# Performance work log

Measured on AMD Instinct MI355X. Metric: run time of the kernel, lower is better.

Reference implementation:

```python
import jax, jax.numpy as jnp
import numpy as np

B, S, H, D = 256, 512, 512, 1  # batch, seq_len, rnn_hid_size (== S*D), input_dim


def lstm_cell(x, h, c, Wih, Whh, bih, bhh):
    # torch.nn.LSTMCell: gates ordered i, f, g, o
    g = x @ Wih.T + bih + h @ Whh.T + bhh  # [B, 4H]
    i, f, gg, o = jnp.split(g, 4, axis=-1)
    i = jax.nn.sigmoid(i)
    f = jax.nn.sigmoid(f)
    gg = jnp.tanh(gg)
    o = jax.nn.sigmoid(o)
    c_new = f * c + i * gg
    h_new = o * jnp.tanh(c_new)
    return h_new, c_new


def setup_inputs() -> dict:
    key = jax.random.key(0)
    ks = jax.random.split(key, 14)
    sc = 1.0 / np.sqrt(H)  # torch LSTMCell/Linear default uniform bound
    u = lambda k, shape: jax.random.uniform(k, shape, jnp.float32, -sc, sc)
    values = jax.random.normal(ks[0], (B, S), jnp.float32)
    masks = jax.random.randint(ks[1], (B, S), 0, 2).astype(jnp.float32)
    return {
        "values": values,
        "masks": masks,
        "Wih_f": u(ks[2], (4 * H, D)), "Whh_f": u(ks[3], (4 * H, H)),
        "bih_f": u(ks[4], (4 * H,)), "bhh_f": u(ks[5], (4 * H,)),
        "Wih_b": u(ks[6], (4 * H, D)), "Whh_b": u(ks[7], (4 * H, H)),
        "bih_b": u(ks[8], (4 * H,)), "bhh_b": u(ks[9], (4 * H,)),
        "W_imp": u(ks[10], (D, H)), "b_imp": u(ks[11], (D,)),
    }


def reference(values, masks, Wih_f, Whh_f, bih_f, bhh_f,
              Wih_b, Whh_b, bih_b, bhh_b, W_imp, b_imp):
    x_f = values[:, :, None]  # [B, S, 1]
    m_f = masks[:, :, None]
    # flip over axis 2 (size 1) is a no-op, matching the original exactly
    x_b = jnp.flip(x_f, axis=2)
    m_b = jnp.flip(m_f, axis=2)

    start_f = jnp.full((B, D), 128.0, jnp.float32)
    start_b = jnp.full((B, D), -128.0, jnp.float32)
    z = jnp.zeros((B, H), jnp.float32)
    h_f, c_f = lstm_cell(start_f, z, z, Wih_f, Whh_f, bih_f, bhh_f)
    h_b, c_b = lstm_cell(start_b, z, z, Wih_b, Whh_b, bih_b, bhh_b)

    xs = (jnp.swapaxes(x_f, 0, 1), jnp.swapaxes(m_f, 0, 1),
          jnp.swapaxes(x_b, 0, 1), jnp.swapaxes(m_b, 0, 1))  # [S, B, 1] each

    def step(carry, inp):
        hf, cf, hb, cb = carry
        xf, mf, xb, mb = inp
        imp_f = hf @ W_imp.T + b_imp
        imp_b = hb @ W_imp.T + b_imp
        cc_f = (1.0 - mf) * xf + mf * imp_f
        cc_b = (1.0 - mb) * xb + mb * imp_b
        hf, cf = lstm_cell(cc_f, hf, cf, Wih_f, Whh_f, bih_f, bhh_f)
        hb, cb = lstm_cell(cc_b, hb, cb, Wih_b, Whh_b, bih_b, bhh_b)
        return (hf, cf, hb, cb), None

    (h_f, c_f, h_b, c_b), _ = jax.lax.scan(step, (h_f, c_f, h_b, c_b), xs)
    h = h_f + h_b  # [B, H]
    imputations = h.reshape(B, S, D)  # requires H == S * D
    out = imputations * (1.0 - m_f) + x_f * m_f
    return h, out
```

## Files before the change

kernel.cpp:

```cpp
#include <hip/hip_runtime.h>
#include <stdint.h>

#define B_ 256
#define S_ 512
#define H_ 512

#define XM_STRIDE 513
#define LDS_BYTES 56320

typedef __attribute__((ext_vector_type(4))) float f32x4;
typedef __attribute__((ext_vector_type(4))) int   i32x4;
typedef __attribute__((ext_vector_type(8))) short s16x8;

__device__ __forceinline__ short f2bf(float f) {
    union { float f; uint32_t u; } c; c.f = f;
    uint32_t u = c.u;
    u += 0x7fffu + ((u >> 16) & 1u);
    return (short)(u >> 16);
}
__device__ __forceinline__ float bflo(uint32_t u) { return __builtin_bit_cast(float, u << 16); }
__device__ __forceinline__ float bfhi(uint32_t u) { return __builtin_bit_cast(float, u & 0xffff0000u); }
__device__ __forceinline__ float sig_(float x)  { return 1.0f / (1.0f + __expf(-x)); }
__device__ __forceinline__ float tanh_(float x) { return 1.0f - 2.0f / (1.0f + __expf(2.0f * x)); }

__device__ __forceinline__ uint32_t pklo(uint32_t hi, uint32_t lo) {
    return __builtin_amdgcn_perm(hi, lo, 0x05040100u);
}

__device__ __forceinline__ void load_a8_issue(const void* p, i32x4* a) {
    asm volatile(
        "global_load_dwordx4 %0, %8, off sc0 sc1\n\t"
        "global_load_dwordx4 %1, %8, off offset:16 sc0 sc1\n\t"
        "global_load_dwordx4 %2, %8, off offset:128 sc0 sc1\n\t"
        "global_load_dwordx4 %3, %8, off offset:144 sc0 sc1\n\t"
        "global_load_dwordx4 %4, %8, off offset:256 sc0 sc1\n\t"
        "global_load_dwordx4 %5, %8, off offset:272 sc0 sc1\n\t"
        "global_load_dwordx4 %6, %8, off offset:384 sc0 sc1\n\t"
        "global_load_dwordx4 %7, %8, off offset:400 sc0 sc1"
        : "=&v"(a[0]), "=&v"(a[1]), "=&v"(a[2]), "=&v"(a[3]),
          "=&v"(a[4]), "=&v"(a[5]), "=&v"(a[6]), "=&v"(a[7])
        : "v"(p)
        : "memory");
}
#define AWAIT(imm, x0, x1, x2, x3) \
    asm volatile("s_waitcnt vmcnt(" #imm ")" : "+v"(x0), "+v"(x1), "+v"(x2), "+v"(x3) :: "memory")

__device__ __forceinline__ uint32_t minof8(const i32x4* ar) {
    uint32_t mn = 0xffffffffu;
    #pragma unroll
    for (int j = 0; j < 8; ++j) {
        uint32_t u0 = (uint32_t)ar[j][0], u1 = (uint32_t)ar[j][1];
        uint32_t u2 = (uint32_t)ar[j][2], u3 = (uint32_t)ar[j][3];
        uint32_t m0 = u0 < u1 ? u0 : u1;
        uint32_t m1 = u2 < u3 ? u2 : u3;
        uint32_t mm = m0 < m1 ? m0 : m1;
        mn = mn < mm ? mn : mm;
    }
    return mn;
}

__device__ __forceinline__ void group_revalidate(i32x4* ar, const void* gb, uint32_t tgtv) {
    uint32_t mn = minof8(ar);
    while (__ballot(mn >= tgtv) != ~0ull) {
        __builtin_amdgcn_s_sleep(1);
        load_a8_issue(gb, ar);
        AWAIT(0, ar[0], ar[1], ar[2], ar[3]);
        AWAIT(0, ar[4], ar[5], ar[6], ar[7]);
        mn = minof8(ar);
    }
}

__global__ void __launch_bounds__(128, 1)
lstm_kernel(const float* __restrict__ values, const float* __restrict__ masks,
            const float* __restrict__ Wih_f, const float* __restrict__ Whh_f,
            const float* __restrict__ bih_f, const float* __restrict__ bhh_f,
            const float* __restrict__ Wih_b, const float* __restrict__ Whh_b,
            const float* __restrict__ bih_b, const float* __restrict__ bhh_b,
            const float* __restrict__ W_imp, const float* __restrict__ b_imp,
            uint32_t* h_buf, float* hfin)
{
    extern __shared__ char smem_raw[];
    short*    imp_lds = (short*)smem_raw;
    uint32_t* xm_lds  = (uint32_t*)(smem_raw + 16384);

    const int tid  = threadIdx.x;
    const int lane = tid & 63;
    const int nw   = tid >> 6;

    const int bid = blockIdx.x;
    const int g   = bid & 15;
    const int w   = (bid >> 4) & 15;
    const int d   = bid >> 8;

    const float* Whh = d ? Whh_b : Whh_f;
    const float* Wih = d ? Wih_b : Wih_f;
    const float* bih = d ? bih_b : bih_f;
    const float* bhh = d ? bhh_b : bhh_f;

    const int col16 = lane & 15;
    const int koff4 = lane >> 4;
    const int jcol  = w * 32 + nw * 16 + col16;

    for (int c = tid; c < 1024; c += 128) {
        int ckoff = (c >> 4) & 3, ckb = c >> 6;
        int k0 = ckb * 32 + ckoff * 8;
        short* dst = &imp_lds[c * 8];
        #pragma unroll
        for (int j = 0; j < 8; ++j) dst[j] = f2bf(W_imp[k0 + j]);
    }
    for (int i = tid; i < 16 * 512; i += 128) {
        int r = i >> 9, s = i & 511;
        float x = values[(g * 16 + r) * S_ + s];
        float m = masks[(g * 16 + r) * S_ + s];
        float a = x * (1.0f - m);
        xm_lds[r * XM_STRIDE + s] =
            (uint32_t)(uint16_t)f2bf(a) | ((uint32_t)(uint16_t)f2bf(m) << 16);
    }

    s16x8 bfr[4][16];
    {
        const float* base = Whh + (size_t)jcol * 512 + koff4 * 8;
        #pragma unroll
        for (int gg = 0; gg < 4; ++gg) {
            const float* src = base + (size_t)gg * 512 * 512;
            #pragma unroll
            for (int kb = 0; kb < 16; ++kb) {
                f32x4 v0 = *(const f32x4*)(src + kb * 32);
                f32x4 v1 = *(const f32x4*)(src + kb * 32 + 4);
                s16x8 b;
                b[0] = f2bf(v0[0]); b[1] = f2bf(v0[1]); b[2] = f2bf(v0[2]); b[3] = f2bf(v0[3]);
                b[4] = f2bf(v1[0]); b[5] = f2bf(v1[1]); b[6] = f2bf(v1[2]); b[7] = f2bf(v1[3]);
                bfr[gg][kb] = b;
            }
        }
    }

    float bias[4], wih[4];
    #pragma unroll
    for (int gg = 0; gg < 4; ++gg) {
        int gc = gg * 512 + jcol;
        bias[gg] = bih[gc] + bhh[gc];
        wih[gg]  = Wih[gc];
    }
    const float bimp  = b_imp[0];
    const float start = d ? -128.0f : 128.0f;

    const int arow    = g * 16 + col16;
    const int rowloc  = koff4 * 4;
    const int rowbase = g * 16 + rowloc;
    const int imp_off = (koff4 * 16 + col16) * 8;

    __syncthreads();

    float c_reg[4];
    {
        float pre[4];
        #pragma unroll
        for (int gg = 0; gg < 4; ++gg) pre[gg] = start * wih[gg] + bias[gg];
        float i0 = sig_(pre[0]), g0 = tanh_(pre[2]), o0 = sig_(pre[3]);
        float c0 = i0 * g0;
        float h0 = o0 * tanh_(c0);
        #pragma unroll
        for (int r = 0; r < 4; ++r) c_reg[r] = c0;
        uint32_t dwi = (1u << 16) | (uint32_t)(uint16_t)f2bf(h0);
        char* dst = (char*)(h_buf + (size_t)d * (B_ * H_) + (size_t)rowbase * H_ + jcol);
        #pragma unroll
        for (int r = 0; r < 4; ++r)
            asm volatile("global_store_dword %0, %1, off sc0 sc1"
                         :: "v"(dst + r * 2048), "v"(dwi) : "memory");
    }

    for (int t = 0; t < S_; ++t) {
        const int p = t & 1;
        const uint32_t* hb_r = h_buf + (size_t)p       * (2 * B_ * H_) + (size_t)d * (B_ * H_);
        uint32_t*       hb_w = h_buf + (size_t)(p ^ 1) * (2 * B_ * H_) + (size_t)d * (B_ * H_);

        const uint32_t tgtv = (uint32_t)(t + 1) << 16;

        {
            const uint32_t* cp = hb_r + (size_t)(g * 16) * H_ + (lane & 31) * 16;
            for (;;) {
                uint32_t f;
                asm volatile("global_load_dword %0, %1, off sc0 sc1\n\ts_waitcnt vmcnt(0)"
                             : "=v"(f) : "v"(cp) : "memory");
                if (__ballot(f >= tgtv) == ~0ull) break;
                __builtin_amdgcn_s_sleep(2);
            }
        }

        const char* ab = (const char*)(hb_r + (size_t)arow * H_ + koff4 * 8);
        i32x4 ar0[8], ar1[8], ar2[8], ar3[8];
        load_a8_issue(ab,        ar0);
        load_a8_issue(ab + 512,  ar1);
        load_a8_issue(ab + 1024, ar2);
        load_a8_issue(ab + 1536, ar3);

        f32x4 acc0 = {0,0,0,0}, acc1 = {0,0,0,0}, acc2 = {0,0,0,0}, acc3 = {0,0,0,0};
        f32x4 acc4 = {0,0,0,0};

        #define PACK_MFMA(G, AR)                                                   \
            _Pragma("unroll")                                                      \
            for (int kk = 0; kk < 4; ++kk) {                                       \
                i32x4 pk;                                                          \
                pk[0] = (int)pklo((uint32_t)AR[2*kk  ][1], (uint32_t)AR[2*kk  ][0]); \
                pk[1] = (int)pklo((uint32_t)AR[2*kk  ][3], (uint32_t)AR[2*kk  ][2]); \
                pk[2] = (int)pklo((uint32_t)AR[2*kk+1][1], (uint32_t)AR[2*kk+1][0]); \
                pk[3] = (int)pklo((uint32_t)AR[2*kk+1][3], (uint32_t)AR[2*kk+1][2]); \
                s16x8 a = __builtin_bit_cast(s16x8, pk);                           \
                const int kb = (G) * 4 + kk;                                       \
                acc0 = __builtin_amdgcn_mfma_f32_16x16x32_bf16(a, bfr[0][kb], acc0, 0, 0, 0); \
                acc1 = __builtin_amdgcn_mfma_f32_16x16x32_bf16(a, bfr[1][kb], acc1, 0, 0, 0); \
                acc2 = __builtin_amdgcn_mfma_f32_16x16x32_bf16(a, bfr[2][kb], acc2, 0, 0, 0); \
                acc3 = __builtin_amdgcn_mfma_f32_16x16x32_bf16(a, bfr[3][kb], acc3, 0, 0, 0); \
                s16x8 b4 = *(const s16x8*)&imp_lds[kb * 512 + imp_off];            \
                acc4 = __builtin_amdgcn_mfma_f32_16x16x32_bf16(a, b4, acc4, 0, 0, 0); \
            }

        AWAIT(24, ar0[0], ar0[1], ar0[2], ar0[3]);
        AWAIT(24, ar0[4], ar0[5], ar0[6], ar0[7]);
        group_revalidate(ar0, ab, tgtv);
        PACK_MFMA(0, ar0)

        AWAIT(16, ar1[0], ar1[1], ar1[2], ar1[3]);
        AWAIT(16, ar1[4], ar1[5], ar1[6], ar1[7]);
        group_revalidate(ar1, ab + 512, tgtv);
        PACK_MFMA(1, ar1)

        AWAIT(8, ar2[0], ar2[1], ar2[2], ar2[3]);
        AWAIT(8, ar2[4], ar2[5], ar2[6], ar2[7]);
        group_revalidate(ar2, ab + 1024, tgtv);
        PACK_MFMA(2, ar2)

        AWAIT(0, ar3[0], ar3[1], ar3[2], ar3[3]);
        AWAIT(0, ar3[4], ar3[5], ar3[6], ar3[7]);
        group_revalidate(ar3, ab + 1536, tgtv);
        PACK_MFMA(3, ar3)
        #undef PACK_MFMA

        const uint32_t tagw = (uint32_t)(t + 2) << 16;
        char* ps = (char*)(hb_w + (size_t)rowbase * H_ + jcol);
        #pragma unroll
        for (int r = 0; r < 4; ++r) {
            uint32_t pk = xm_lds[(rowloc + r) * XM_STRIDE + t];
            float cc = bflo(pk) + bfhi(pk) * (acc4[r] + bimp);
            float pi = acc0[r] + cc * wih[0] + bias[0];
            float pf = acc1[r] + cc * wih[1] + bias[1];
            float pg = acc2[r] + cc * wih[2] + bias[2];
            float po = acc3[r] + cc * wih[3] + bias[3];
            float iv = sig_(pi), fv = sig_(pf), gv = tanh_(pg), ov = sig_(po);
            c_reg[r] = fv * c_reg[r] + iv * gv;
            float hn = ov * tanh_(c_reg[r]);
            uint32_t dw = tagw | (uint32_t)(uint16_t)f2bf(hn);
            asm volatile("global_store_dword %0, %1, off sc0 sc1"
                         :: "v"(ps + r * 2048), "v"(dw) : "memory");
            if (t == S_ - 1) hfin[d * (B_ * H_) + (rowbase + r) * H_ + jcol] = hn;
        }
    }
}

__global__ void __launch_bounds__(256)
epilogue_kernel(const float* __restrict__ values, const float* __restrict__ masks,
                const float* __restrict__ hfin, float* __restrict__ out)
{
    int i = blockIdx.x * 256 + threadIdx.x;
    float h = hfin[i] + hfin[B_ * H_ + i];
    float xv = values[i], mv = masks[i];
    float blend = h * (1.0f - mv) + xv * mv;
    out[i] = h;
    out[B_ * H_ + i] = blend;
}

extern "C" void kernel_launch(void* const* d_in, const int* in_sizes, int n_in,
                              void* d_out, int out_size, void* d_ws, size_t ws_size,
                              hipStream_t stream) {
    const float* values = (const float*)d_in[0];
    const float* masks  = (const float*)d_in[1];
    const float* Wih_f  = (const float*)d_in[2];
    const float* Whh_f  = (const float*)d_in[3];
    const float* bih_f  = (const float*)d_in[4];
    const float* bhh_f  = (const float*)d_in[5];
    const float* Wih_b  = (const float*)d_in[6];
    const float* Whh_b  = (const float*)d_in[7];
    const float* bih_b  = (const float*)d_in[8];
    const float* bhh_b  = (const float*)d_in[9];
    const float* W_imp  = (const float*)d_in[10];
    const float* b_imp  = (const float*)d_in[11];

    uint32_t* h_buf = (uint32_t*)d_ws;
    float*    hfin  = (float*)d_out;

    hipMemsetAsync(d_ws, 0, (size_t)2 * 2 * B_ * H_ * 4, stream);

    hipFuncSetAttribute((const void*)lstm_kernel,
                        hipFuncAttributeMaxDynamicSharedMemorySize, LDS_BYTES);

    void* args[] = {
        (void*)&values, (void*)&masks,
        (void*)&Wih_f, (void*)&Whh_f, (void*)&bih_f, (void*)&bhh_f,
        (void*)&Wih_b, (void*)&Whh_b, (void*)&bih_b, (void*)&bhh_b,
        (void*)&W_imp, (void*)&b_imp,
        (void*)&h_buf, (void*)&hfin
    };
    hipError_t err = hipLaunchCooperativeKernel((const void*)lstm_kernel,
                                                dim3(512), dim3(128), args,
                                                (unsigned int)LDS_BYTES, stream);
    if (err != hipSuccess) {
        lstm_kernel<<<dim3(512), dim3(128), LDS_BYTES, stream>>>(
            values, masks, Wih_f, Whh_f, bih_f, bhh_f,
            Wih_b, Whh_b, bih_b, bhh_b, W_imp, b_imp, h_buf, hfin);
    }

    epilogue_kernel<<<dim3((B_ * H_) / 256), dim3(256), 0, stream>>>(
        values, masks, hfin, (float*)d_out);
}
```

Baseline: 2.318 ms.

## Map LSTM clusters onto single XCDs and use L2-scoped loads/stores when co-located

Block indices are remapped so the 16 workgroups sharing a batch-group cluster are meant to land on the same XCD, assuming round-robin dispatch of blocks across the 8 XCDs. At startup each block publishes its XCC_ID to a flag array, and the cluster checks whether all members share one XCD. If they do, the per-step h exchange uses sc0-only loads and stores that stay coherent through the shared L2, avoiding the system-coherent (sc0 sc1) path. Otherwise it falls back to the original coherent path, at the cost of an extra handshake and a duplicated templated scan loop.

```diff
diff --git a/kernel.cpp b/kernel.cpp
--- a/kernel.cpp
+++ b/kernel.cpp
@@ -27,7 +27,7 @@
     return __builtin_amdgcn_perm(hi, lo, 0x05040100u);
 }
 
-__device__ __forceinline__ void load_a8_issue(const void* p, i32x4* a) {
+__device__ __forceinline__ void load_a8_llc(const void* p, i32x4* a) {
     asm volatile(
         "global_load_dwordx4 %0, %8, off sc0 sc1\n\t"
         "global_load_dwordx4 %1, %8, off offset:16 sc0 sc1\n\t"
@@ -39,8 +39,43 @@
         "global_load_dwordx4 %7, %8, off offset:400 sc0 sc1"
         : "=&v"(a[0]), "=&v"(a[1]), "=&v"(a[2]), "=&v"(a[3]),
           "=&v"(a[4]), "=&v"(a[5]), "=&v"(a[6]), "=&v"(a[7])
-        : "v"(p)
-        : "memory");
+        : "v"(p) : "memory");
+}
+__device__ __forceinline__ void load_a8_l2(const void* p, i32x4* a) {
+    asm volatile(
+        "global_load_dwordx4 %0, %8, off sc0\n\t"
+        "global_load_dwordx4 %1, %8, off offset:16 sc0\n\t"
+        "global_load_dwordx4 %2, %8, off offset:128 sc0\n\t"
+        "global_load_dwordx4 %3, %8, off offset:144 sc0\n\t"
+        "global_load_dwordx4 %4, %8, off offset:256 sc0\n\t"
+        "global_load_dwordx4 %5, %8, off offset:272 sc0\n\t"
+        "global_load_dwordx4 %6, %8, off offset:384 sc0\n\t"
+        "global_load_dwordx4 %7, %8, off offset:400 sc0"
+        : "=&v"(a[0]), "=&v"(a[1]), "=&v"(a[2]), "=&v"(a[3]),
+          "=&v"(a[4]), "=&v"(a[5]), "=&v"(a[6]), "=&v"(a[7])
+        : "v"(p) : "memory");
+}
+template <bool FAST>
+__device__ __forceinline__ void load_a8(const void* p, i32x4* a) {
+    if constexpr (FAST) load_a8_l2(p, a); else load_a8_llc(p, a);
+}
+template <bool FAST>
+__device__ __forceinline__ void store_dw(void* p, uint32_t v) {
+    if constexpr (FAST)
+        asm volatile("global_store_dword %0, %1, off sc0" :: "v"(p), "v"(v) : "memory");
+    else
+        asm volatile("global_store_dword %0, %1, off sc0 sc1" :: "v"(p), "v"(v) : "memory");
+}
+template <bool FAST>
+__device__ __forceinline__ uint32_t canary_ld(const void* p) {
+    uint32_t f;
+    if constexpr (FAST)
+        asm volatile("global_load_dword %0, %1, off sc0\n\ts_waitcnt vmcnt(0)"
+                     : "=v"(f) : "v"(p) : "memory");
+    else
+        asm volatile("global_load_dword %0, %1, off sc0 sc1\n\ts_waitcnt vmcnt(0)"
+                     : "=v"(f) : "v"(p) : "memory");
+    return f;
 }
 #define AWAIT(imm, x0, x1, x2, x3) \
     asm volatile("s_waitcnt vmcnt(" #imm ")" : "+v"(x0), "+v"(x1), "+v"(x2), "+v"(x3) :: "memory")
@@ -58,17 +93,19 @@
     }
     return mn;
 }
-
+template <bool FAST>
 __device__ __forceinline__ void group_revalidate(i32x4* ar, const void* gb, uint32_t tgtv) {
     uint32_t mn = minof8(ar);
     while (__ballot(mn >= tgtv) != ~0ull) {
         __builtin_amdgcn_s_sleep(1);
-        load_a8_issue(gb, ar);
+        load_a8<FAST>(gb, ar);
         AWAIT(0, ar[0], ar[1], ar[2], ar[3]);
         AWAIT(0, ar[4], ar[5], ar[6], ar[7]);
         mn = minof8(ar);
     }
 }
+
+template <bool B> struct BoolT { static constexpr bool value = B; };
 
 __global__ void __launch_bounds__(128, 1)
 lstm_kernel(const float* __restrict__ values, const float* __restrict__ masks,
@@ -77,20 +114,27 @@
             const float* __restrict__ Wih_b, const float* __restrict__ Whh_b,
             const float* __restrict__ bih_b, const float* __restrict__ bhh_b,
             const float* __restrict__ W_imp, const float* __restrict__ b_imp,
-            uint32_t* h_buf, float* hfin)
+            unsigned int* ctrs, uint32_t* h_buf, float* hfin)
 {
     extern __shared__ char smem_raw[];
-    short*    imp_lds = (short*)smem_raw;
-    uint32_t* xm_lds  = (uint32_t*)(smem_raw + 16384);
+    short*        imp_lds  = (short*)smem_raw;
+    uint32_t*     xm_lds   = (uint32_t*)(smem_raw + 16384);
+    volatile int* mode_lds = (volatile int*)(smem_raw + 49216);
+
+    uint32_t* flags = (uint32_t*)ctrs + 64;
 
     const int tid  = threadIdx.x;
     const int lane = tid & 63;
     const int nw   = tid >> 6;
 
     const int bid = blockIdx.x;
-    const int g   = bid & 15;
-    const int w   = (bid >> 4) & 15;
-    const int d   = bid >> 8;
+    const int x   = bid & 7;
+    const int k   = bid >> 3;
+    const int c2  = ((k >> 5) << 1) | (k & 1);
+    const int w   = (k >> 1) & 15;
+    const int cluster = x * 4 + c2;
+    const int d   = cluster >> 4;
+    const int g   = cluster & 15;
 
     const float* Whh = d ? Whh_b : Whh_f;
     const float* Wih = d ? Wih_b : Wih_f;
@@ -101,6 +145,10 @@
     const int koff4 = lane >> 4;
     const int jcol  = w * 32 + nw * 16 + col16;
 
+    uint32_t xcc;
+    asm volatile("s_getreg_b32 %0, hwreg(HW_REG_XCC_ID)" : "=s"(xcc));
+    xcc &= 0xfu;
+
     for (int c = tid; c < 1024; c += 128) {
         int ckoff = (c >> 4) & 3, ckb = c >> 6;
         int k0 = ckb * 32 + ckoff * 8;
@@ -110,11 +158,11 @@
     }
     for (int i = tid; i < 16 * 512; i += 128) {
         int r = i >> 9, s = i & 511;
-        float x = values[(g * 16 + r) * S_ + s];
-        float m = masks[(g * 16 + r) * S_ + s];
-        float a = x * (1.0f - m);
+        float xv = values[(g * 16 + r) * S_ + s];
+        float mv = masks[(g * 16 + r) * S_ + s];
+        float a = xv * (1.0f - mv);
         xm_lds[r * XM_STRIDE + s] =
-            (uint32_t)(uint16_t)f2bf(a) | ((uint32_t)(uint16_t)f2bf(m) << 16);
+            (uint32_t)(uint16_t)f2bf(a) | ((uint32_t)(uint16_t)f2bf(mv) << 16);
     }
 
     s16x8 bfr[4][16];
@@ -150,6 +198,9 @@
     const int rowbase = g * 16 + rowloc;
     const int imp_off = (koff4 * 16 + col16) * 8;
 
+    uint32_t*       myflag = flags + cluster * 16 + w;
+    const uint32_t* pollp  = flags + cluster * 16 + col16;
+
     __syncthreads();
 
     float c_reg[4];
@@ -166,96 +217,116 @@
         char* dst = (char*)(h_buf + (size_t)d * (B_ * H_) + (size_t)rowbase * H_ + jcol);
         #pragma unroll
         for (int r = 0; r < 4; ++r)
-            asm volatile("global_store_dword %0, %1, off sc0 sc1"
-                         :: "v"(dst + r * 2048), "v"(dwi) : "memory");
-    }
-
-    for (int t = 0; t < S_; ++t) {
-        const int p = t & 1;
-        const uint32_t* hb_r = h_buf + (size_t)p       * (2 * B_ * H_) + (size_t)d * (B_ * H_);
-        uint32_t*       hb_w = h_buf + (size_t)(p ^ 1) * (2 * B_ * H_) + (size_t)d * (B_ * H_);
-
-        const uint32_t tgtv = (uint32_t)(t + 1) << 16;
-
-        {
-            const uint32_t* cp = hb_r + (size_t)(g * 16) * H_ + (lane & 31) * 16;
-            for (;;) {
-                uint32_t f;
-                asm volatile("global_load_dword %0, %1, off sc0 sc1\n\ts_waitcnt vmcnt(0)"
-                             : "=v"(f) : "v"(cp) : "memory");
-                if (__ballot(f >= tgtv) == ~0ull) break;
-                __builtin_amdgcn_s_sleep(2);
+            store_dw<false>(dst + r * 2048, dwi);
+    }
+    asm volatile("s_waitcnt vmcnt(0)" ::: "memory");
+    __syncthreads();
+    if (tid == 0)
+        asm volatile("global_store_dword %0, %1, off sc0 sc1"
+                     :: "v"(myflag), "v"((xcc << 8) | 1u) : "memory");
+
+    if (nw == 0) {
+        uint32_t f;
+        for (;;) {
+            asm volatile("global_load_dword %0, %1, off sc0 sc1\n\ts_waitcnt vmcnt(0)"
+                         : "=v"(f) : "v"(pollp) : "memory");
+            if (__ballot((f & 0xffu) >= 1u) == ~0ull) break;
+            __builtin_amdgcn_s_sleep(2);
+        }
+        if (lane == 0)
+            *mode_lds = (__ballot((f >> 8) == xcc) == ~0ull) ? 1 : 0;
+    }
+    __syncthreads();
+    const int fastu = __builtin_amdgcn_readfirstlane(*mode_lds);
+
+    auto scan = [&](auto FC) {
+        constexpr bool F = decltype(FC)::value;
+        for (int t = 0; t < S_; ++t) {
+            const int p = t & 1;
+            const uint32_t* hb_r = h_buf + (size_t)p       * (2 * B_ * H_) + (size_t)d * (B_ * H_);
+            uint32_t*       hb_w = h_buf + (size_t)(p ^ 1) * (2 * B_ * H_) + (size_t)d * (B_ * H_);
+
+            const uint32_t tgtv = (uint32_t)(t + 1) << 16;
+
+            {
+                const uint32_t* cp = hb_r + (size_t)(g * 16) * H_ + (lane & 31) * 16;
+                for (;;) {
+                    uint32_t f = canary_ld<F>(cp);
+                    if (__ballot(f >= tgtv) == ~0ull) break;
+                    __builtin_amdgcn_s_sleep(2);
+                }
+            }
+
+            const char* ab = (const char*)(hb_r + (size_t)arow * H_ + koff4 * 8);
+            i32x4 ar0[8], ar1[8], ar2[8], ar3[8];
+            load_a8<F>(ab,        ar0);
+            load_a8<F>(ab + 512,  ar1);
+            load_a8<F>(ab + 1024, ar2);
+            load_a8<F>(ab + 1536, ar3);
+
+            f32x4 acc0 = {0,0,0,0}, acc1 = {0,0,0,0}, acc2 = {0,0,0,0}, acc3 = {0,0,0,0};
+            f32x4 acc4 = {0,0,0,0};
+
+            #define PACK_MFMA(G, AR)                                                   \
+                _Pragma("unroll")                                                      \
+                for (int kk = 0; kk < 4; ++kk) {                                       \
+                    i32x4 pk;                                                          \
+                    pk[0] = (int)pklo((uint32_t)AR[2*kk  ][1], (uint32_t)AR[2*kk  ][0]); \
+                    pk[1] = (int)pklo((uint32_t)AR[2*kk  ][3], (uint32_t)AR[2*kk  ][2]); \
+                    pk[2] = (int)pklo((uint32_t)AR[2*kk+1][1], (uint32_t)AR[2*kk+1][0]); \
+                    pk[3] = (int)pklo((uint32_t)AR[2*kk+1][3], (uint32_t)AR[2*kk+1][2]); \
+                    s16x8 a = __builtin_bit_cast(s16x8, pk);                           \
+                    const int kb = (G) * 4 + kk;                                       \
+                    acc0 = __builtin_amdgcn_mfma_f32_16x16x32_bf16(a, bfr[0][kb], acc0, 0, 0, 0); \
+                    acc1 = __builtin_amdgcn_mfma_f32_16x16x32_bf16(a, bfr[1][kb], acc1, 0, 0, 0); \
+                    acc2 = __builtin_amdgcn_mfma_f32_16x16x32_bf16(a, bfr[2][kb], acc2, 0, 0, 0); \
+                    acc3 = __builtin_amdgcn_mfma_f32_16x16x32_bf16(a, bfr[3][kb], acc3, 0, 0, 0); \
+                    s16x8 b4 = *(const s16x8*)&imp_lds[kb * 512 + imp_off];            \
+                    acc4 = __builtin_amdgcn_mfma_f32_16x16x32_bf16(a, b4, acc4, 0, 0, 0); \
+                }
+
+            AWAIT(24, ar0[0], ar0[1], ar0[2], ar0[3]);
+            AWAIT(24, ar0[4], ar0[5], ar0[6], ar0[7]);
+            group_revalidate<F>(ar0, ab, tgtv);
+            PACK_MFMA(0, ar0)
+
+            AWAIT(16, ar1[0], ar1[1], ar1[2], ar1[3]);
+            AWAIT(16, ar1[4], ar1[5], ar1[6], ar1[7]);
+            group_revalidate<F>(ar1, ab + 512, tgtv);
+            PACK_MFMA(1, ar1)
+
+            AWAIT(8, ar2[0], ar2[1], ar2[2], ar2[3]);
+            AWAIT(8, ar2[4], ar2[5], ar2[6], ar2[7]);
+            group_revalidate<F>(ar2, ab + 1024, tgtv);
+            PACK_MFMA(2, ar2)
+
+            AWAIT(0, ar3[0], ar3[1], ar3[2], ar3[3]);
+            AWAIT(0, ar3[4], ar3[5], ar3[6], ar3[7]);
+            group_revalidate<F>(ar3, ab + 1536, tgtv);
+            PACK_MFMA(3, ar3)
+            #undef PACK_MFMA
+
+            const uint32_t tagw = (uint32_t)(t + 2) << 16;
+            char* ps = (char*)(hb_w + (size_t)rowbase * H_ + jcol);
+            #pragma unroll
+            for (int r = 0; r < 4; ++r) {
+                uint32_t pk = xm_lds[(rowloc + r) * XM_STRIDE + t];
+                float cc = bflo(pk) + bfhi(pk) * (acc4[r] + bimp);
+                float pi = acc0[r] + cc * wih[0] + bias[0];
+                float pf = acc1[r] + cc * wih[1] + bias[1];
+                float pg = acc2[r] + cc * wih[2] + bias[2];
+                float po = acc3[r] + cc * wih[3] + bias[3];
+                float iv = sig_(pi), fv = sig_(pf), gv = tanh_(pg), ov = sig_(po);
+                c_reg[r] = fv * c_reg[r] + iv * gv;
+                float hn = ov * tanh_(c_reg[r]);
+                uint32_t dw = tagw | (uint32_t)(uint16_t)f2bf(hn);
+                store_dw<F>(ps + r * 2048, dw);
+                if (t == S_ - 1) hfin[d * (B_ * H_) + (rowbase + r) * H_ + jcol] = hn;
             }
         }
-
-        const char* ab = (const char*)(hb_r + (size_t)arow * H_ + koff4 * 8);
-        i32x4 ar0[8], ar1[8], ar2[8], ar3[8];
-        load_a8_issue(ab,        ar0);
-        load_a8_issue(ab + 512,  ar1);
-        load_a8_issue(ab + 1024, ar2);
-        load_a8_issue(ab + 1536, ar3);
-
-        f32x4 acc0 = {0,0,0,0}, acc1 = {0,0,0,0}, acc2 = {0,0,0,0}, acc3 = {0,0,0,0};
-        f32x4 acc4 = {0,0,0,0};
-
-        #define PACK_MFMA(G, AR)                                                   \
-            _Pragma("unroll")                                                      \
-            for (int kk = 0; kk < 4; ++kk) {                                       \
-                i32x4 pk;                                                          \
-                pk[0] = (int)pklo((uint32_t)AR[2*kk  ][1], (uint32_t)AR[2*kk  ][0]); \
-                pk[1] = (int)pklo((uint32_t)AR[2*kk  ][3], (uint32_t)AR[2*kk  ][2]); \
-                pk[2] = (int)pklo((uint32_t)AR[2*kk+1][1], (uint32_t)AR[2*kk+1][0]); \
-                pk[3] = (int)pklo((uint32_t)AR[2*kk+1][3], (uint32_t)AR[2*kk+1][2]); \
-                s16x8 a = __builtin_bit_cast(s16x8, pk);                           \
-                const int kb = (G) * 4 + kk;                                       \
-                acc0 = __builtin_amdgcn_mfma_f32_16x16x32_bf16(a, bfr[0][kb], acc0, 0, 0, 0); \
-                acc1 = __builtin_amdgcn_mfma_f32_16x16x32_bf16(a, bfr[1][kb], acc1, 0, 0, 0); \
-                acc2 = __builtin_amdgcn_mfma_f32_16x16x32_bf16(a, bfr[2][kb], acc2, 0, 0, 0); \
-                acc3 = __builtin_amdgcn_mfma_f32_16x16x32_bf16(a, bfr[3][kb], acc3, 0, 0, 0); \
-                s16x8 b4 = *(const s16x8*)&imp_lds[kb * 512 + imp_off];            \
-                acc4 = __builtin_amdgcn_mfma_f32_16x16x32_bf16(a, b4, acc4, 0, 0, 0); \
-            }
-
-        AWAIT(24, ar0[0], ar0[1], ar0[2], ar0[3]);
-        AWAIT(24, ar0[4], ar0[5], ar0[6], ar0[7]);
-        group_revalidate(ar0, ab, tgtv);
-        PACK_MFMA(0, ar0)
-
-        AWAIT(16, ar1[0], ar1[1], ar1[2], ar1[3]);
-        AWAIT(16, ar1[4], ar1[5], ar1[6], ar1[7]);
-        group_revalidate(ar1, ab + 512, tgtv);
-        PACK_MFMA(1, ar1)
-
-        AWAIT(8, ar2[0], ar2[1], ar2[2], ar2[3]);
-        AWAIT(8, ar2[4], ar2[5], ar2[6], ar2[7]);
-        group_revalidate(ar2, ab + 1024, tgtv);
-        PACK_MFMA(2, ar2)
-
-        AWAIT(0, ar3[0], ar3[1], ar3[2], ar3[3]);
-        AWAIT(0, ar3[4], ar3[5], ar3[6], ar3[7]);
-        group_revalidate(ar3, ab + 1536, tgtv);
-        PACK_MFMA(3, ar3)
-        #undef PACK_MFMA
-
-        const uint32_t tagw = (uint32_t)(t + 2) << 16;
-        char* ps = (char*)(hb_w + (size_t)rowbase * H_ + jcol);
-        #pragma unroll
-        for (int r = 0; r < 4; ++r) {
-            uint32_t pk = xm_lds[(rowloc + r) * XM_STRIDE + t];
-            float cc = bflo(pk) + bfhi(pk) * (acc4[r] + bimp);
-            float pi = acc0[r] + cc * wih[0] + bias[0];
-            float pf = acc1[r] + cc * wih[1] + bias[1];
-            float pg = acc2[r] + cc * wih[2] + bias[2];
-            float po = acc3[r] + cc * wih[3] + bias[3];
-            float iv = sig_(pi), fv = sig_(pf), gv = tanh_(pg), ov = sig_(po);
-            c_reg[r] = fv * c_reg[r] + iv * gv;
-            float hn = ov * tanh_(c_reg[r]);
-            uint32_t dw = tagw | (uint32_t)(uint16_t)f2bf(hn);
-            asm volatile("global_store_dword %0, %1, off sc0 sc1"
-                         :: "v"(ps + r * 2048), "v"(dw) : "memory");
-            if (t == S_ - 1) hfin[d * (B_ * H_) + (rowbase + r) * H_ + jcol] = hn;
-        }
-    }
+    };
+    if (fastu) scan(BoolT<true>{});
+    else       scan(BoolT<false>{});
 }
 
 __global__ void __launch_bounds__(256)
@@ -286,10 +357,11 @@
     const float* W_imp  = (const float*)d_in[10];
     const float* b_imp  = (const float*)d_in[11];
 
-    uint32_t* h_buf = (uint32_t*)d_ws;
-    float*    hfin  = (float*)d_out;
-
-    hipMemsetAsync(d_ws, 0, (size_t)2 * 2 * B_ * H_ * 4, stream);
+    unsigned int* ctrs  = (unsigned int*)d_ws;
+    uint32_t*     h_buf = (uint32_t*)((char*)d_ws + 8192);
+    float*        hfin  = (float*)d_out;
+
+    hipMemsetAsync(d_ws, 0, 8192 + (size_t)2 * 2 * B_ * H_ * 4, stream);
 
     hipFuncSetAttribute((const void*)lstm_kernel,
                         hipFuncAttributeMaxDynamicSharedMemorySize, LDS_BYTES);
@@ -299,7 +371,7 @@
         (void*)&Wih_f, (void*)&Whh_f, (void*)&bih_f, (void*)&bhh_f,
         (void*)&Wih_b, (void*)&Whh_b, (void*)&bih_b, (void*)&bhh_b,
         (void*)&W_imp, (void*)&b_imp,
-        (void*)&h_buf, (void*)&hfin
+        (void*)&ctrs, (void*)&h_buf, (void*)&hfin
     };
     hipError_t err = hipLaunchCooperativeKernel((const void*)lstm_kernel,
                                                 dim3(512), dim3(128), args,
@@ -307,7 +379,7 @@
     if (err != hipSuccess) {
         lstm_kernel<<<dim3(512), dim3(128), LDS_BYTES, stream>>>(
             values, masks, Wih_f, Whh_f, bih_f, bhh_f,
-            Wih_b, Whh_b, bih_b, bhh_b, W_imp, b_imp, h_buf, hfin);
+            Wih_b, Whh_b, bih_b, bhh_b, W_imp, b_imp, ctrs, h_buf, hfin);
     }
 
     epilogue_kernel<<<dim3((B_ * H_) / 256), dim3(256), 0, stream>>>(
```

New measurement: 3.387 ms. 46.1% more time.
